# Performance work log

Measured on AMD Instinct MI355X. Metric: run time of the kernel, lower is better.

The kernel has to match this reference:

```python
import jax, jax.numpy as jnp
import numpy as np

BN_EPS = 1e-5
STRIDE = 4
K_NEAREST = 16


def _fps(xyz, m):
    """Farthest point sampling. xyz: [n,3] -> indices [m] (seeded at point 0)."""
    n = xyz.shape[0]

    def body(i, state):
        dist, idxs, last = state
        d = jnp.sum((xyz - xyz[last]) ** 2, axis=-1)
        dist = jnp.minimum(dist, d)
        nxt = jnp.argmax(dist).astype(jnp.int32)
        return dist, idxs.at[i].set(nxt), nxt

    init = (jnp.full((n,), 1e10, xyz.dtype), jnp.zeros((m,), jnp.int32), jnp.int32(0))
    _, idxs, _ = jax.lax.fori_loop(1, m, body, init)
    return idxs


def _knn(q, x, k):
    """q: [m,3] queries, x: [n,3] points -> [m,k] nearest-neighbor indices."""
    d = jnp.sum((q[:, None, :] - x[None, :, :]) ** 2, axis=-1)  # [m,n]
    _, idx = jax.lax.top_k(-d, k)
    return idx


def setup_inputs() -> dict:
    key = jax.random.key(0)
    k0, k1, k2 = jax.random.split(key, 3)
    B, N, IN_CH, OUT_CH = 4, 8192, 64, 128
    events = jax.random.uniform(k0, (B, N, 4), dtype=jnp.float32)  # xyz in [0,1) + time
    features = jax.random.normal(k1, (B, N, IN_CH), dtype=jnp.float32)
    W = jax.random.normal(k2, (4 + IN_CH, OUT_CH), dtype=jnp.float32) / np.float32(np.sqrt(4 + IN_CH))
    b = jnp.zeros((OUT_CH,), jnp.float32)
    gamma = jnp.ones((OUT_CH,), jnp.float32)
    beta = jnp.zeros((OUT_CH,), jnp.float32)
    return dict(events=events, features=features, W=W, b=b, gamma=gamma, beta=beta)


def reference(events, features, W, b, gamma, beta):
    B, N, _ = events.shape
    m = N // STRIDE  # down_offsets = offsets // stride with equal-size samples
    xyz = events[..., :3]
    xyz_c = jax.lax.stop_gradient(xyz)  # indices are non-differentiable

    # farthest point sampling per cloud -> [B, m]
    down_idx = jax.vmap(lambda p: _fps(p, m))(xyz_c)
    down_xyz = jnp.take_along_axis(xyz_c, down_idx[..., None], axis=1)  # [B,m,3]
    # k nearest neighbors of each sampled point -> [B, m, K]
    idx = jax.vmap(lambda q, x: _knn(q, x, K_NEAREST))(down_xyz, xyz_c)

    down_events = jnp.take_along_axis(events, down_idx[..., None], axis=1)  # [B,m,4]
    grouped_events = jax.vmap(lambda e, i: e[i])(events, idx)               # [B,m,K,4]
    grouped_events_norm = grouped_events - down_events[:, :, None, :]
    grouped_features = jax.vmap(lambda f, i: f[i])(features, idx)           # [B,m,K,in_ch]
    g = jnp.concatenate([grouped_events_norm, grouped_features], axis=-1)   # [B,m,K,4+in_ch]

    # Linear -> BatchNorm1d (training batch stats over all points & neighbors) -> ReLU
    h = jnp.einsum('bmkc,cd->bmkd', g, W) + b
    mu = jnp.mean(h, axis=(0, 1, 2))
    var = jnp.var(h, axis=(0, 1, 2))
    h = (h - mu) * jax.lax.rsqrt(var + BN_EPS) * gamma + beta
    h = jax.nn.relu(h)

    down_features = jnp.max(h, axis=2)  # max-pool over K neighbors -> [B,m,out_ch]
    return down_events, down_features
```

## Files before the change

kernel.cpp:

```cpp
#include <hip/hip_runtime.h>

#define N_PTS 8192
#define M_PTS 2048
#define K_NN 16
#define IN_CH 64
#define G_CH 68
#define OUT_CH 128
#define KCAP 128

__device__ __forceinline__ float subrn(float a, float b) {
    float r; asm("v_sub_f32 %0, %1, %2" : "=v"(r) : "v"(a), "v"(b)); return r;
}
__device__ __forceinline__ float mulrn(float a, float b) {
    float r; asm("v_mul_f32 %0, %1, %2" : "=v"(r) : "v"(a), "v"(b)); return r;
}
__device__ __forceinline__ float addrn(float a, float b) {
    float r; asm("v_add_f32 %0, %1, %2" : "=v"(r) : "v"(a), "v"(b)); return r;
}
__device__ __forceinline__ float sqdist_rn(float ax, float ay, float az,
                                           float bx, float by, float bz) {
    float dx = subrn(ax, bx);
    float dy = subrn(ay, by);
    float dz = subrn(az, bz);
    return addrn(addrn(mulrn(dx, dx), mulrn(dy, dy)), mulrn(dz, dz));
}

typedef float v2f __attribute__((ext_vector_type(2)));
__device__ __forceinline__ v2f pk_add(v2f a, v2f b) {
    v2f r; asm("v_pk_add_f32 %0, %1, %2" : "=v"(r) : "v"(a), "v"(b)); return r;
}
__device__ __forceinline__ v2f pk_mul(v2f a, v2f b) {
    v2f r; asm("v_pk_mul_f32 %0, %1, %2" : "=v"(r) : "v"(a), "v"(b)); return r;
}

template <int CTRL>
__device__ __forceinline__ float movdpp_f(float x) {
    int r = __builtin_amdgcn_mov_dpp(__float_as_int(x), CTRL, 0xf, 0xf, true);
    return __int_as_float(r);
}
template <int CTRL>
__device__ __forceinline__ int movdpp_i(int x) {
    return __builtin_amdgcn_mov_dpp(x, CTRL, 0xf, 0xf, true);
}
template <int CTRL, int RM>
__device__ __forceinline__ float dppmaxf_m(float x) {
    int r = __builtin_amdgcn_update_dpp(0, __float_as_int(x), CTRL, RM, 0xf, false);
    return fmaxf(x, __int_as_float(r));
}
__device__ __forceinline__ float wave_max64(float x) {
    x = fmaxf(x, movdpp_f<0xB1>(x));
    x = fmaxf(x, movdpp_f<0x4E>(x));
    x = fmaxf(x, movdpp_f<0x141>(x));
    x = fmaxf(x, movdpp_f<0x140>(x));
    x = dppmaxf_m<0x142, 0xa>(x);
    x = dppmaxf_m<0x143, 0xc>(x);
    return x;
}
__device__ __forceinline__ float group8_max(float x) {
    x = fmaxf(x, movdpp_f<0xB1>(x));
    x = fmaxf(x, movdpp_f<0x4E>(x));
    x = fmaxf(x, movdpp_f<0x141>(x));
    return x;
}
__device__ __forceinline__ int group8_min_i(int x) {
    x = min(x, movdpp_i<0xB1>(x));
    x = min(x, movdpp_i<0x4E>(x));
    x = min(x, movdpp_i<0x141>(x));
    return x;
}

__global__ __launch_bounds__(512) void fps_kernel(const float4* __restrict__ events4,
                                                  int* __restrict__ down_idx,
                                                  float4* __restrict__ out_de) {
    extern __shared__ char smem[];
    float*  rv   = (float*)smem;
    int*    wsl  = (int*)(smem + 32);
    int*    ssel = (int*)(smem + 64);
    float4* spt  = (float4*)(smem + 64 + 4 * M_PTS);

    const int b = blockIdx.x;
    const int tid = threadIdx.x;
    const int wave = tid >> 6;
    const int lane = tid & 63;
    const float4* ev = events4 + (size_t)b * N_PTS;

    for (int i = tid; i < N_PTS; i += 512) spt[i] = ev[i];
    if (tid == 0) ssel[0] = 0;
    __syncthreads();

    v2f px[8], py[8], pz[8];
    float dist[16];
#pragma unroll
    for (int pp = 0; pp < 8; ++pp) {
        float4 f0 = spt[tid * 16 + 2 * pp];
        float4 f1 = spt[tid * 16 + 2 * pp + 1];
        px[pp] = (v2f){f0.x, f1.x};
        py[pp] = (v2f){f0.y, f1.y};
        pz[pp] = (v2f){f0.z, f1.z};
        dist[2 * pp] = 1e10f; dist[2 * pp + 1] = 1e10f;
    }

    int last = 0;
    for (int i = 1; i < M_PTS; ++i) {
        float4 L = spt[last];
        const float nlx = -L.x, nly = -L.y, nlz = -L.z;
        const v2f nx2 = (v2f){nlx, nlx};
        const v2f ny2 = (v2f){nly, nly};
        const v2f nz2 = (v2f){nlz, nlz};
#pragma unroll
        for (int pp = 0; pp < 8; ++pp) {
            v2f dx = pk_add(px[pp], nx2);
            v2f dy = pk_add(py[pp], ny2);
            v2f dz = pk_add(pz[pp], nz2);
            v2f s  = pk_add(pk_add(pk_mul(dx, dx), pk_mul(dy, dy)), pk_mul(dz, dz));
            dist[2 * pp]     = fminf(dist[2 * pp],     s.x);
            dist[2 * pp + 1] = fminf(dist[2 * pp + 1], s.y);
        }
        float m0 = fmaxf(dist[0], dist[1]),  m1 = fmaxf(dist[2], dist[3]);
        float m2 = fmaxf(dist[4], dist[5]),  m3 = fmaxf(dist[6], dist[7]);
        float m4 = fmaxf(dist[8], dist[9]),  m5 = fmaxf(dist[10], dist[11]);
        float m6 = fmaxf(dist[12], dist[13]), m7 = fmaxf(dist[14], dist[15]);
        m0 = fmaxf(m0, m1); m2 = fmaxf(m2, m3); m4 = fmaxf(m4, m5); m6 = fmaxf(m6, m7);
        float bd = fmaxf(fmaxf(m0, m2), fmaxf(m4, m6));

        float wm = wave_max64(bd);
        if (lane == 63) rv[wave] = wm;
        __syncthreads();
        float bm = group8_max(rv[lane & 7]);

        bool cand = (bd == bm);
        unsigned long long mask = __ballot(cand);
        if (lane == 0) wsl[wave] = 0x7fffffff;
        if (mask != 0ULL) {
            int fl = (int)__ffsll((long long)mask) - 1;
            if (lane == fl) {
                int jm = 0;
#pragma unroll
                for (int j = 15; j >= 0; --j) if (dist[j] == bd) jm = j;
                wsl[wave] = tid * 16 + jm;
            }
        }
        __syncthreads();
        int winner = group8_min_i(wsl[lane & 7]);
        if (tid == 0) ssel[i] = winner;
        last = winner;
    }
    __syncthreads();

    for (int i = tid; i < M_PTS; i += 512) {
        int s = ssel[i];
        down_idx[b * M_PTS + i] = s;
        out_de[(size_t)b * M_PTS + i] = spt[s];
    }
}

__global__ __launch_bounds__(256) void knn_kernel(const float4* __restrict__ events4,
                                                  const int* __restrict__ down_idx,
                                                  int* __restrict__ knn_idx) {
    extern __shared__ char smem[];
    float* sx   = (float*)smem;
    float* sy   = sx + N_PTS;
    float* sz   = sy + N_PTS;
    float* cd   = sz + N_PTS;
    int*   ci   = (int*)(cd + 32 * KCAP);
    int*   scnt = (int*)(ci + 32 * KCAP);

    const int b    = blockIdx.x >> 6;
    const int qg   = blockIdx.x & 63;
    const int tid  = threadIdx.x;
    const int ql   = tid >> 3;
    const int part = tid & 7;

    const float4* ev = events4 + (size_t)b * N_PTS;
    for (int i = tid; i < N_PTS; i += 256) {
        float4 e = ev[i];
        sx[i] = e.x; sy[i] = e.y; sz[i] = e.z;
    }
    if (tid < 32) scnt[tid] = 0;
    __syncthreads();

    const int q  = qg * 32 + ql;
    const int qi = down_idx[b * M_PTS + q];
    const float qx = sx[qi], qy = sy[qi], qz = sz[qi];

    float m1 = 1e30f, m2 = 1e30f;
    for (int i = 0; i < N_PTS / 8; ++i) {
        const int p = i * 8 + part;
        float d = sqdist_rn(sx[p], sy[p], sz[p], qx, qy, qz);
        float lo = fminf(m1, d);
        m2 = fminf(m2, fmaxf(m1, d));
        m1 = lo;
    }
    const float T = group8_max(m2);

    for (int i = 0; i < N_PTS / 8; ++i) {
        const int p = i * 8 + part;
        float d = sqdist_rn(sx[p], sy[p], sz[p], qx, qy, qz);
        if (d <= T) {
            int pos = atomicAdd(&scnt[ql], 1);
            if (pos < KCAP) { cd[ql * KCAP + pos] = d; ci[ql * KCAP + pos] = p; }
        }
    }
    __syncthreads();

    if (part == 0) {
        float nd[16]; int ni[16];
#pragma unroll
        for (int j = 0; j < 16; ++j) { nd[j] = 1e30f; ni[j] = 0x7fffffff; }
        float wmax = 1e30f; int widx = 0x7fffffff; int wslot = 0;
        const int n = scnt[ql];
        const int lim = (n <= KCAP) ? n : 0;
        for (int t = 0; t < lim; ++t) {
            float d = cd[ql * KCAP + t];
            int   p = ci[ql * KCAP + t];
            if (d < wmax || (d == wmax && p < widx)) {
#pragma unroll
                for (int j = 0; j < 16; ++j) if (j == wslot) { nd[j] = d; ni[j] = p; }
                float m_ = -1.0f; int mix_ = -1; int ms_ = 0;
#pragma unroll
                for (int j = 0; j < 16; ++j)
                    if (nd[j] > m_ || (nd[j] == m_ && ni[j] > mix_)) { m_ = nd[j]; mix_ = ni[j]; ms_ = j; }
                wmax = m_; widx = mix_; wslot = ms_;
            }
        }
        if (n > KCAP) {
            for (int p = 0; p < N_PTS; ++p) {
                float d = sqdist_rn(sx[p], sy[p], sz[p], qx, qy, qz);
                if (d < wmax || (d == wmax && p < widx)) {
#pragma unroll
                    for (int j = 0; j < 16; ++j) if (j == wslot) { nd[j] = d; ni[j] = p; }
                    float m_ = -1.0f; int mix_ = -1; int ms_ = 0;
#pragma unroll
                    for (int j = 0; j < 16; ++j)
                        if (nd[j] > m_ || (nd[j] == m_ && ni[j] > mix_)) { m_ = nd[j]; mix_ = ni[j]; ms_ = j; }
                    wmax = m_; widx = mix_; wslot = ms_;
                }
            }
        }
        int* out = knn_idx + ((size_t)(b * M_PTS + q)) * K_NN;
#pragma unroll
        for (int j = 0; j < 16; ++j) out[j] = ni[j];
    }
}

__global__ __launch_bounds__(256) void gmm_kernel(const float* __restrict__ events,
                                                  const float* __restrict__ features,
                                                  const float* __restrict__ W,
                                                  const float* __restrict__ bias,
                                                  const int* __restrict__ knn_idx,
                                                  const float* __restrict__ de,
                                                  float* __restrict__ hmax_g,
                                                  float* __restrict__ hmin_g,
                                                  float* __restrict__ gsum,
                                                  float* __restrict__ gsq) {
    __shared__ __align__(16) float sg[16 * G_CH];
    __shared__ float scomb[2 * OUT_CH];

    const int b   = blockIdx.x >> 7;
    const int qg  = blockIdx.x & 127;
    const int tid = threadIdx.x;
    const int d   = tid & 127;
    const int kh  = tid >> 7;

    float w[G_CH];
#pragma unroll
    for (int c = 0; c < G_CH; ++c) w[c] = W[c * OUT_CH + d];
    const float breg = bias[d];

    float ssum = 0.f, ssq = 0.f;
    const float4* sg4 = (const float4*)sg;

    for (int qq = 0; qq < 16; ++qq) {
        const int q = qg * 16 + qq;
        const int base = b * M_PTS + q;
        for (int j = tid; j < 16 * G_CH; j += 256) {
            int k = j / G_CH;
            int c = j - k * G_CH;
            int nb = knn_idx[base * K_NN + k];
            float v;
            if (c < 4) v = events[((size_t)(b * N_PTS + nb)) * 4 + c] - de[(size_t)base * 4 + c];
            else       v = features[((size_t)(b * N_PTS + nb)) * IN_CH + (c - 4)];
            sg[j] = v;
        }
        __syncthreads();

        float hmax = -1e30f, hmin = 1e30f;
#pragma unroll
        for (int k2 = 0; k2 < 8; ++k2) {
            const int k = kh * 8 + k2;
            float acc = breg;
#pragma unroll
            for (int c4 = 0; c4 < 17; ++c4) {
                float4 g = sg4[k * 17 + c4];
                acc = fmaf(g.x, w[4 * c4 + 0], acc);
                acc = fmaf(g.y, w[4 * c4 + 1], acc);
                acc = fmaf(g.z, w[4 * c4 + 2], acc);
                acc = fmaf(g.w, w[4 * c4 + 3], acc);
            }
            hmax = fmaxf(hmax, acc);
            hmin = fminf(hmin, acc);
            ssum += acc;
            ssq = fmaf(acc, acc, ssq);
        }
        if (kh == 1) { scomb[d] = hmax; scomb[OUT_CH + d] = hmin; }
        __syncthreads();
        if (kh == 0) {
            hmax = fmaxf(hmax, scomb[d]);
            hmin = fminf(hmin, scomb[OUT_CH + d]);
            hmax_g[(size_t)base * OUT_CH + d] = hmax;
            hmin_g[(size_t)base * OUT_CH + d] = hmin;
        }
        __syncthreads();
    }
    if (kh == 1) { scomb[d] = ssum; scomb[OUT_CH + d] = ssq; }
    __syncthreads();
    if (kh == 0) {
        atomicAdd(&gsum[d], ssum + scomb[d]);
        atomicAdd(&gsq[d],  ssq  + scomb[OUT_CH + d]);
    }
}

__global__ __launch_bounds__(256) void fin_kernel(const float* __restrict__ hmax_g,
                                                  const float* __restrict__ hmin_g,
                                                  const float* __restrict__ gsum,
                                                  const float* __restrict__ gsq,
                                                  const float* __restrict__ gamma,
                                                  const float* __restrict__ beta,
                                                  float* __restrict__ out) {
    const size_t e = (size_t)blockIdx.x * 256 + threadIdx.x;
    const int d = (int)(e & 127);
    const float inv_cnt = 1.0f / 131072.0f;
    float mu  = gsum[d] * inv_cnt;
    float var = gsq[d] * inv_cnt - mu * mu;
    float a   = gamma[d] * rsqrtf(var + 1e-5f);
    float sh  = fmaf(-mu, a, beta[d]);
    float hv  = (a >= 0.f) ? hmax_g[e] : hmin_g[e];
    float r   = fmaf(a, hv, sh);
    out[32768 + e] = r > 0.f ? r : 0.f;
}

extern "C" void kernel_launch(void* const* d_in, const int* in_sizes, int n_in,
                              void* d_out, int out_size, void* d_ws, size_t ws_size,
                              hipStream_t stream) {
    const float* events   = (const float*)d_in[0];
    const float* features = (const float*)d_in[1];
    const float* W        = (const float*)d_in[2];
    const float* bias     = (const float*)d_in[3];
    const float* gamma    = (const float*)d_in[4];
    const float* beta     = (const float*)d_in[5];
    float* out = (float*)d_out;
    char* ws = (char*)d_ws;

    int*   down_idx = (int*)ws;
    int*   knn_idx  = (int*)(ws + 32768);
    float* gsum     = (float*)(ws + 32768 + 524288);
    float* gsq      = gsum + OUT_CH;
    float* hmaxg    = (float*)(ws + 558080);
    float* hming    = hmaxg + (size_t)4 * M_PTS * OUT_CH;

    (void)hipMemsetAsync(gsum, 0, 2 * OUT_CH * sizeof(float), stream);

    const size_t fps_lds = 64 + 4 * M_PTS + (size_t)N_PTS * sizeof(float4);
    fps_kernel<<<4, 512, fps_lds, stream>>>((const float4*)events, down_idx, (float4*)out);

    const size_t knn_lds = (size_t)3 * N_PTS * sizeof(float)
                         + (size_t)32 * KCAP * 8 + 128;
    knn_kernel<<<256, 256, knn_lds, stream>>>((const float4*)events, down_idx, knn_idx);

    gmm_kernel<<<512, 256, 0, stream>>>(events, features, W, bias, knn_idx, out,
                                        hmaxg, hming, gsum, gsq);

    fin_kernel<<<4096, 256, 0, stream>>>(hmaxg, hming, gsum, gsq, gamma, beta, out);
}
```

Measured before the change: 2.443 ms.

## Shrink FPS block to four waves and pick argmax winner with LDS atomicMin

```diff
diff --git a/kernel.cpp b/kernel.cpp
--- a/kernel.cpp
+++ b/kernel.cpp
@@ -37,10 +37,6 @@
 __device__ __forceinline__ float movdpp_f(float x) {
     int r = __builtin_amdgcn_mov_dpp(__float_as_int(x), CTRL, 0xf, 0xf, true);
     return __int_as_float(r);
-}
-template <int CTRL>
-__device__ __forceinline__ int movdpp_i(int x) {
-    return __builtin_amdgcn_mov_dpp(x, CTRL, 0xf, 0xf, true);
 }
 template <int CTRL, int RM>
 __device__ __forceinline__ float dppmaxf_m(float x) {
@@ -56,27 +52,26 @@
     x = dppmaxf_m<0x143, 0xc>(x);
     return x;
 }
+__device__ __forceinline__ float group4_max(float x) {
+    x = fmaxf(x, movdpp_f<0xB1>(x));
+    x = fmaxf(x, movdpp_f<0x4E>(x));
+    return x;
+}
 __device__ __forceinline__ float group8_max(float x) {
     x = fmaxf(x, movdpp_f<0xB1>(x));
     x = fmaxf(x, movdpp_f<0x4E>(x));
     x = fmaxf(x, movdpp_f<0x141>(x));
     return x;
 }
-__device__ __forceinline__ int group8_min_i(int x) {
-    x = min(x, movdpp_i<0xB1>(x));
-    x = min(x, movdpp_i<0x4E>(x));
-    x = min(x, movdpp_i<0x141>(x));
-    return x;
-}
-
-__global__ __launch_bounds__(512) void fps_kernel(const float4* __restrict__ events4,
+
+__global__ __launch_bounds__(256) void fps_kernel(const float4* __restrict__ events4,
                                                   int* __restrict__ down_idx,
                                                   float4* __restrict__ out_de) {
     extern __shared__ char smem[];
     float*  rv   = (float*)smem;
-    int*    wsl  = (int*)(smem + 32);
-    int*    ssel = (int*)(smem + 64);
-    float4* spt  = (float4*)(smem + 64 + 4 * M_PTS);
+    int*    wsl  = (int*)(smem + 16);
+    int*    ssel = (int*)(smem + 32);
+    float4* spt  = (float4*)(smem + 32 + 4 * M_PTS);
 
     const int b = blockIdx.x;
     const int tid = threadIdx.x;
@@ -84,16 +79,16 @@
     const int lane = tid & 63;
     const float4* ev = events4 + (size_t)b * N_PTS;
 
-    for (int i = tid; i < N_PTS; i += 512) spt[i] = ev[i];
-    if (tid == 0) ssel[0] = 0;
-    __syncthreads();
-
-    v2f px[8], py[8], pz[8];
-    float dist[16];
-#pragma unroll
-    for (int pp = 0; pp < 8; ++pp) {
-        float4 f0 = spt[tid * 16 + 2 * pp];
-        float4 f1 = spt[tid * 16 + 2 * pp + 1];
+    for (int i = tid; i < N_PTS; i += 256) spt[i] = ev[i];
+    if (tid == 0) { ssel[0] = 0; wsl[0] = 0x7fffffff; wsl[1] = 0x7fffffff; }
+    __syncthreads();
+
+    v2f px[16], py[16], pz[16];
+    float dist[32];
+#pragma unroll
+    for (int pp = 0; pp < 16; ++pp) {
+        float4 f0 = spt[(2 * pp) * 256 + tid];
+        float4 f1 = spt[(2 * pp + 1) * 256 + tid];
         px[pp] = (v2f){f0.x, f1.x};
         py[pp] = (v2f){f0.y, f1.y};
         pz[pp] = (v2f){f0.z, f1.z};
@@ -108,7 +103,7 @@
         const v2f ny2 = (v2f){nly, nly};
         const v2f nz2 = (v2f){nlz, nlz};
 #pragma unroll
-        for (int pp = 0; pp < 8; ++pp) {
+        for (int pp = 0; pp < 16; ++pp) {
             v2f dx = pk_add(px[pp], nx2);
             v2f dy = pk_add(py[pp], ny2);
             v2f dz = pk_add(pz[pp], nz2);
@@ -116,38 +111,33 @@
             dist[2 * pp]     = fminf(dist[2 * pp],     s.x);
             dist[2 * pp + 1] = fminf(dist[2 * pp + 1], s.y);
         }
-        float m0 = fmaxf(dist[0], dist[1]),  m1 = fmaxf(dist[2], dist[3]);
-        float m2 = fmaxf(dist[4], dist[5]),  m3 = fmaxf(dist[6], dist[7]);
-        float m4 = fmaxf(dist[8], dist[9]),  m5 = fmaxf(dist[10], dist[11]);
-        float m6 = fmaxf(dist[12], dist[13]), m7 = fmaxf(dist[14], dist[15]);
-        m0 = fmaxf(m0, m1); m2 = fmaxf(m2, m3); m4 = fmaxf(m4, m5); m6 = fmaxf(m6, m7);
-        float bd = fmaxf(fmaxf(m0, m2), fmaxf(m4, m6));
+        float t0[16];
+#pragma unroll
+        for (int j = 0; j < 16; ++j) t0[j] = fmaxf(dist[2 * j], dist[2 * j + 1]);
+#pragma unroll
+        for (int j = 0; j < 8; ++j) t0[j] = fmaxf(t0[2 * j], t0[2 * j + 1]);
+#pragma unroll
+        for (int j = 0; j < 4; ++j) t0[j] = fmaxf(t0[2 * j], t0[2 * j + 1]);
+        float bd = fmaxf(fmaxf(t0[0], t0[1]), fmaxf(t0[2], t0[3]));
 
         float wm = wave_max64(bd);
         if (lane == 63) rv[wave] = wm;
         __syncthreads();
-        float bm = group8_max(rv[lane & 7]);
-
-        bool cand = (bd == bm);
-        unsigned long long mask = __ballot(cand);
-        if (lane == 0) wsl[wave] = 0x7fffffff;
-        if (mask != 0ULL) {
-            int fl = (int)__ffsll((long long)mask) - 1;
-            if (lane == fl) {
-                int jm = 0;
-#pragma unroll
-                for (int j = 15; j >= 0; --j) if (dist[j] == bd) jm = j;
-                wsl[wave] = tid * 16 + jm;
-            }
-        }
-        __syncthreads();
-        int winner = group8_min_i(wsl[lane & 7]);
-        if (tid == 0) ssel[i] = winner;
-        last = winner;
-    }
-    __syncthreads();
-
-    for (int i = tid; i < M_PTS; i += 512) {
+        float bm = group4_max(rv[lane & 3]);
+
+        if (bd == bm) {
+            int jm = 0;
+#pragma unroll
+            for (int j = 31; j >= 0; --j) if (dist[j] == bd) jm = j;
+            atomicMin(&wsl[i & 1], jm * 256 + tid);
+        }
+        __syncthreads();
+        last = wsl[i & 1];
+        if (tid == 0) { ssel[i] = last; wsl[(i + 1) & 1] = 0x7fffffff; }
+    }
+    __syncthreads();
+
+    for (int i = tid; i < M_PTS; i += 256) {
         int s = ssel[i];
         down_idx[b * M_PTS + i] = s;
         out_de[(size_t)b * M_PTS + i] = spt[s];
@@ -360,8 +350,8 @@
 
     (void)hipMemsetAsync(gsum, 0, 2 * OUT_CH * sizeof(float), stream);
 
-    const size_t fps_lds = 64 + 4 * M_PTS + (size_t)N_PTS * sizeof(float4);
-    fps_kernel<<<4, 512, fps_lds, stream>>>((const float4*)events, down_idx, (float4*)out);
+    const size_t fps_lds = 32 + 4 * M_PTS + (size_t)N_PTS * sizeof(float4);
+    fps_kernel<<<4, 256, fps_lds, stream>>>((const float4*)events, down_idx, (float4*)out);
 
     const size_t knn_lds = (size_t)3 * N_PTS * sizeof(float)
                          + (size_t)32 * KCAP * 8 + 128;
```

Result: slower. 2.797 ms (+14.5%).

## Fuse FPS argmax into one barrier per iteration with packed (dist,idx) reduction

Applied to the files above, without the earlier changes.

```diff
diff --git a/kernel.cpp b/kernel.cpp
--- a/kernel.cpp
+++ b/kernel.cpp
@@ -46,6 +46,11 @@
 __device__ __forceinline__ float dppmaxf_m(float x) {
     int r = __builtin_amdgcn_update_dpp(0, __float_as_int(x), CTRL, RM, 0xf, false);
     return fmaxf(x, __int_as_float(r));
+}
+template <int CTRL, int RM>
+__device__ __forceinline__ int dppmini_m(int x) {
+    int r = __builtin_amdgcn_update_dpp(0x7fffffff, x, CTRL, RM, 0xf, false);
+    return min(x, r);
 }
 __device__ __forceinline__ float wave_max64(float x) {
     x = fmaxf(x, movdpp_f<0xB1>(x));
@@ -56,27 +61,29 @@
     x = dppmaxf_m<0x143, 0xc>(x);
     return x;
 }
+__device__ __forceinline__ int wave_min64_i(int x) {
+    x = min(x, movdpp_i<0xB1>(x));
+    x = min(x, movdpp_i<0x4E>(x));
+    x = min(x, movdpp_i<0x141>(x));
+    x = min(x, movdpp_i<0x140>(x));
+    x = dppmini_m<0x142, 0xa>(x);
+    x = dppmini_m<0x143, 0xc>(x);
+    return x;
+}
 __device__ __forceinline__ float group8_max(float x) {
     x = fmaxf(x, movdpp_f<0xB1>(x));
     x = fmaxf(x, movdpp_f<0x4E>(x));
     x = fmaxf(x, movdpp_f<0x141>(x));
     return x;
 }
-__device__ __forceinline__ int group8_min_i(int x) {
-    x = min(x, movdpp_i<0xB1>(x));
-    x = min(x, movdpp_i<0x4E>(x));
-    x = min(x, movdpp_i<0x141>(x));
-    return x;
-}
 
 __global__ __launch_bounds__(512) void fps_kernel(const float4* __restrict__ events4,
                                                   int* __restrict__ down_idx,
                                                   float4* __restrict__ out_de) {
     extern __shared__ char smem[];
-    float*  rv   = (float*)smem;
-    int*    wsl  = (int*)(smem + 32);
-    int*    ssel = (int*)(smem + 64);
-    float4* spt  = (float4*)(smem + 64 + 4 * M_PTS);
+    int2*   rp   = (int2*)smem;
+    int*    ssel = (int*)(smem + 128);
+    float4* spt  = (float4*)(smem + 128 + 4 * M_PTS);
 
     const int b = blockIdx.x;
     const int tid = threadIdx.x;
@@ -92,8 +99,8 @@
     float dist[16];
 #pragma unroll
     for (int pp = 0; pp < 8; ++pp) {
-        float4 f0 = spt[tid * 16 + 2 * pp];
-        float4 f1 = spt[tid * 16 + 2 * pp + 1];
+        float4 f0 = spt[(2 * pp) * 512 + tid];
+        float4 f1 = spt[(2 * pp + 1) * 512 + tid];
         px[pp] = (v2f){f0.x, f1.x};
         py[pp] = (v2f){f0.y, f1.y};
         pz[pp] = (v2f){f0.z, f1.z};
@@ -116,34 +123,43 @@
             dist[2 * pp]     = fminf(dist[2 * pp],     s.x);
             dist[2 * pp + 1] = fminf(dist[2 * pp + 1], s.y);
         }
-        float m0 = fmaxf(dist[0], dist[1]),  m1 = fmaxf(dist[2], dist[3]);
-        float m2 = fmaxf(dist[4], dist[5]),  m3 = fmaxf(dist[6], dist[7]);
-        float m4 = fmaxf(dist[8], dist[9]),  m5 = fmaxf(dist[10], dist[11]);
-        float m6 = fmaxf(dist[12], dist[13]), m7 = fmaxf(dist[14], dist[15]);
-        m0 = fmaxf(m0, m1); m2 = fmaxf(m2, m3); m4 = fmaxf(m4, m5); m6 = fmaxf(m6, m7);
-        float bd = fmaxf(fmaxf(m0, m2), fmaxf(m4, m6));
+        float t0[8];
+#pragma unroll
+        for (int j = 0; j < 8; ++j) t0[j] = fmaxf(dist[2 * j], dist[2 * j + 1]);
+#pragma unroll
+        for (int j = 0; j < 4; ++j) t0[j] = fmaxf(t0[2 * j], t0[2 * j + 1]);
+        float bd = fmaxf(fmaxf(t0[0], t0[1]), fmaxf(t0[2], t0[3]));
 
         float wm = wave_max64(bd);
-        if (lane == 63) rv[wave] = wm;
+        float wmb = __int_as_float(__builtin_amdgcn_readlane(__float_as_int(wm), 63));
+
+        int myidx = 0x7fffffff;
+        if (bd == wmb) {
+            int jm = 0;
+#pragma unroll
+            for (int j = 15; j >= 0; --j) if (dist[j] == bd) jm = j;
+            myidx = jm * 512 + tid;
+        }
+        int wmin = wave_min64_i(myidx);
+
+        if (lane == 63) rp[(i & 1) * 8 + wave] = make_int2(__float_as_int(wmb), wmin);
         __syncthreads();
-        float bm = group8_max(rv[lane & 7]);
-
-        bool cand = (bd == bm);
-        unsigned long long mask = __ballot(cand);
-        if (lane == 0) wsl[wave] = 0x7fffffff;
-        if (mask != 0ULL) {
-            int fl = (int)__ffsll((long long)mask) - 1;
-            if (lane == fl) {
-                int jm = 0;
-#pragma unroll
-                for (int j = 15; j >= 0; --j) if (dist[j] == bd) jm = j;
-                wsl[wave] = tid * 16 + jm;
-            }
-        }
-        __syncthreads();
-        int winner = group8_min_i(wsl[lane & 7]);
-        if (tid == 0) ssel[i] = winner;
-        last = winner;
+
+        int2 pr = rp[(i & 1) * 8 + (lane & 7)];
+        int db = pr.x, ib = pr.y;
+        {
+            int od = movdpp_i<0xB1>(db), oi = movdpp_i<0xB1>(ib);
+            bool t = (od > db) || (od == db && oi < ib);
+            db = t ? od : db; ib = t ? oi : ib;
+            od = movdpp_i<0x4E>(db); oi = movdpp_i<0x4E>(ib);
+            t = (od > db) || (od == db && oi < ib);
+            db = t ? od : db; ib = t ? oi : ib;
+            od = movdpp_i<0x141>(db); oi = movdpp_i<0x141>(ib);
+            t = (od > db) || (od == db && oi < ib);
+            db = t ? od : db; ib = t ? oi : ib;
+        }
+        last = ib;
+        if (tid == 0) ssel[i] = last;
     }
     __syncthreads();
 
@@ -360,7 +376,7 @@
 
     (void)hipMemsetAsync(gsum, 0, 2 * OUT_CH * sizeof(float), stream);
 
-    const size_t fps_lds = 64 + 4 * M_PTS + (size_t)N_PTS * sizeof(float4);
+    const size_t fps_lds = 128 + 4 * M_PTS + (size_t)N_PTS * sizeof(float4);
     fps_kernel<<<4, 512, fps_lds, stream>>>((const float4*)events, down_idx, (float4*)out);
 
     const size_t knn_lds = (size_t)3 * N_PTS * sizeof(float)
```

Measured after the change: 2.594 ms. +6.2%, slower.
